# Kernel tuning notes

Measured on AMD Instinct MI355X. Metric: run time of the kernel, lower is better.

Reference implementation:

```python
import jax, jax.numpy as jnp
import numpy as np

NUM_NODES = 100000
NUM_REL = 8
HIDDEN = 128
NUM_EDGES = 1600000
NUM_LAYERS = 2


def setup_inputs() -> dict:
    key = jax.random.key(0)
    k1, k2, k3, k4, k5 = jax.random.split(key, 5)
    x = jnp.arange(NUM_NODES, dtype=jnp.int64)
    edge_index = jax.random.randint(k1, (2, NUM_EDGES), 0, NUM_NODES, dtype=jnp.int64)
    edge_type = jax.random.randint(k2, (NUM_EDGES,), 0, NUM_REL, dtype=jnp.int64)
    emb = jax.random.normal(k3, (NUM_NODES, HIDDEN), dtype=jnp.float32) * 0.1
    W = jax.random.normal(k4, (NUM_LAYERS, NUM_REL, HIDDEN, HIDDEN), dtype=jnp.float32) * (1.0 / np.sqrt(HIDDEN))
    root = jax.random.normal(k5, (NUM_LAYERS, HIDDEN, HIDDEN), dtype=jnp.float32) * (1.0 / np.sqrt(HIDDEN))
    bias = jnp.zeros((NUM_LAYERS, HIDDEN), dtype=jnp.float32)
    return {"x": x, "edge_index": edge_index, "edge_type": edge_type,
            "emb": emb, "W": W, "root": root, "bias": bias}


def _rgcn_conv(h, src, dst, etype, W_l, root_l, bias_l):
    # h: [N, d]; W_l: [R, d, d]
    n = h.shape[0]
    r = W_l.shape[0]
    # Transform all nodes by every relation weight: [R, N, d]
    xW = jnp.einsum('nd,rdf->rnf', h, W_l)
    # Per-edge message gathered by (relation, source): [E, d]
    msg = xW[etype, src]
    # Mean-normalize per (target node, relation), matching PyG aggr='mean'
    seg = dst * r + etype  # combined (node, relation) segment id
    cnt = jax.ops.segment_sum(jnp.ones(msg.shape[0], dtype=h.dtype), seg,
                              num_segments=n * r)
    norm = 1.0 / jnp.maximum(cnt[seg], 1.0)
    agg = jax.ops.segment_sum(msg * norm[:, None], dst, num_segments=n)
    return agg + h @ root_l + bias_l


def reference(x, edge_index, edge_type, emb, W, root, bias):
    src, dst = edge_index[0], edge_index[1]
    h = emb[x]  # embedding lookup
    for l in range(NUM_LAYERS):
        h = _rgcn_conv(h, src, dst, edge_type, W[l], root[l], bias[l])
        h = jax.nn.relu(h)
    return h
```

## Files before the change

kernel.cpp:

```cpp
#include <hip/hip_runtime.h>

typedef unsigned int u32;
typedef unsigned short u16;
typedef __attribute__((ext_vector_type(8))) short short8;
typedef __attribute__((ext_vector_type(4))) float f32x4;

#define DD 128
#define RREL 8
#define KCAT 1152
#define NKT 9
#define SCAN_CHUNK 4096

static __device__ __forceinline__ u16 f2bf(float f) {
  u32 u = __builtin_bit_cast(u32, f);
  u32 r = (u + 0x7fffu + ((u >> 16) & 1u)) >> 16;
  return (u16)r;
}
static __device__ __forceinline__ float bflo(u32 v) { return __builtin_bit_cast(float, v << 16); }
static __device__ __forceinline__ float bfhi(u32 v) { return __builtin_bit_cast(float, v & 0xffff0000u); }

__global__ __launch_bounds__(256) void k_convw(const float* __restrict__ W,
                                               const float* __restrict__ root,
                                               uint4* __restrict__ wt) {
  int t = blockIdx.x * 256 + threadIdx.x;
  if (t >= 2 * NKT * 2048) return;
  int l = t / (NKT * 2048);
  int rem = t - l * (NKT * 2048);
  int kt = rem >> 11;
  int pos = rem & 2047;
  int col = pos >> 4;
  int cbx = pos & 15;
  int cb = cbx ^ (col & 7);
  int k0 = kt * DD + cb * 8;
  u16 vals[8];
#pragma unroll
  for (int i = 0; i < 8; ++i) {
    int k = k0 + i;
    float v;
    if (k < DD) {
      v = root[(size_t)l * DD * DD + k * DD + col];
    } else {
      int km = k - DD;
      v = W[((size_t)l * RREL + (km >> 7)) * DD * DD + (size_t)(km & 127) * DD + col];
    }
    vals[i] = f2bf(v);
  }
  wt[t] = *(uint4*)vals;
}

__global__ __launch_bounds__(256) void k_gather(const int* __restrict__ x,
                                                const float* __restrict__ emb,
                                                u16* __restrict__ acat, int N) {
  int t = blockIdx.x * 256 + threadIdx.x;
  if (t >= N * 16) return;
  int node = t >> 4, part = t & 15;
  const float4* e4 = (const float4*)(emb + (size_t)x[node] * DD + part * 8);
  float4 f0 = e4[0], f1 = e4[1];
  uint4 u;
  u.x = (u32)f2bf(f0.x) | ((u32)f2bf(f0.y) << 16);
  u.y = (u32)f2bf(f0.z) | ((u32)f2bf(f0.w) << 16);
  u.z = (u32)f2bf(f1.x) | ((u32)f2bf(f1.y) << 16);
  u.w = (u32)f2bf(f1.z) | ((u32)f2bf(f1.w) << 16);
  *(uint4*)(acat + (size_t)node * KCAT + part * 8) = u;
}

__global__ __launch_bounds__(256) void k_hist(const int* __restrict__ ei,
                                              const int* __restrict__ et,
                                              int* __restrict__ cnt, int E) {
  int base = (blockIdx.x * 256 + threadIdx.x) * 8;
  if (base + 7 < E) {
    int4 dA = *(const int4*)(ei + E + base);
    int4 dB = *(const int4*)(ei + E + base + 4);
    int4 tA = *(const int4*)(et + base);
    int4 tB = *(const int4*)(et + base + 4);
    atomicAdd(&cnt[dA.x * 8 + tA.x], 1);
    atomicAdd(&cnt[dA.y * 8 + tA.y], 1);
    atomicAdd(&cnt[dA.z * 8 + tA.z], 1);
    atomicAdd(&cnt[dA.w * 8 + tA.w], 1);
    atomicAdd(&cnt[dB.x * 8 + tB.x], 1);
    atomicAdd(&cnt[dB.y * 8 + tB.y], 1);
    atomicAdd(&cnt[dB.z * 8 + tB.z], 1);
    atomicAdd(&cnt[dB.w * 8 + tB.w], 1);
  } else {
    for (int e = base; e < E; ++e) atomicAdd(&cnt[ei[E + e] * 8 + et[e]], 1);
  }
}

__global__ __launch_bounds__(256) void k_scan_reduce(const int* __restrict__ cnt,
                                                     int* __restrict__ blksum, int nseg) {
  __shared__ int s[256];
  int b = blockIdx.x, t = threadIdx.x;
  int base = b * SCAN_CHUNK;
  int sum = 0;
  for (int i = 0; i < 16; ++i) {
    int idx = base + i * 256 + t;
    if (idx < nseg) sum += cnt[idx];
  }
  s[t] = sum;
  __syncthreads();
  for (int st = 128; st > 0; st >>= 1) {
    if (t < st) s[t] += s[t + st];
    __syncthreads();
  }
  if (t == 0) blksum[b] = s[0];
}

__global__ void k_scan_top(int* __restrict__ blksum, int nblk, int* __restrict__ off,
                           int nseg, int E) {
  if (threadIdx.x == 0 && blockIdx.x == 0) {
    int run = 0;
    for (int b = 0; b < nblk; ++b) { int v = blksum[b]; blksum[b] = run; run += v; }
    off[nseg] = E;
  }
}

__global__ __launch_bounds__(256) void k_scan_write(const int* __restrict__ cnt,
                                                    const int* __restrict__ blksum,
                                                    int* __restrict__ off, int nseg) {
  __shared__ int s[256];
  int b = blockIdx.x, t = threadIdx.x;
  int base = b * SCAN_CHUNK + t * 16;
  int v[16];
  int sum = 0;
#pragma unroll
  for (int i = 0; i < 16; ++i) {
    int idx = base + i;
    v[i] = (idx < nseg) ? cnt[idx] : 0;
    sum += v[i];
  }
  s[t] = sum;
  __syncthreads();
  for (int st = 1; st < 256; st <<= 1) {
    int add = (t >= st) ? s[t - st] : 0;
    __syncthreads();
    s[t] += add;
    __syncthreads();
  }
  int run = blksum[b] + s[t] - sum;
#pragma unroll
  for (int i = 0; i < 16; ++i) {
    int idx = base + i;
    if (idx < nseg) off[idx] = run;
    run += v[i];
  }
}

__global__ __launch_bounds__(256) void k_scatter(const int* __restrict__ ei,
                                                 const int* __restrict__ et,
                                                 int* __restrict__ fill,
                                                 int* __restrict__ sorted, int E) {
  int base = (blockIdx.x * 256 + threadIdx.x) * 8;
  if (base + 7 < E) {
    int4 sA = *(const int4*)(ei + base);
    int4 sB = *(const int4*)(ei + base + 4);
    int4 dA = *(const int4*)(ei + E + base);
    int4 dB = *(const int4*)(ei + E + base + 4);
    int4 tA = *(const int4*)(et + base);
    int4 tB = *(const int4*)(et + base + 4);
    int p0 = atomicAdd(&fill[dA.x * 8 + tA.x], 1);
    int p1 = atomicAdd(&fill[dA.y * 8 + tA.y], 1);
    int p2 = atomicAdd(&fill[dA.z * 8 + tA.z], 1);
    int p3 = atomicAdd(&fill[dA.w * 8 + tA.w], 1);
    int p4 = atomicAdd(&fill[dB.x * 8 + tB.x], 1);
    int p5 = atomicAdd(&fill[dB.y * 8 + tB.y], 1);
    int p6 = atomicAdd(&fill[dB.z * 8 + tB.z], 1);
    int p7 = atomicAdd(&fill[dB.w * 8 + tB.w], 1);
    sorted[p0] = sA.x;
    sorted[p1] = sA.y;
    sorted[p2] = sA.z;
    sorted[p3] = sA.w;
    sorted[p4] = sB.x;
    sorted[p5] = sB.y;
    sorted[p6] = sB.z;
    sorted[p7] = sB.w;
  } else {
    for (int e = base; e < E; ++e) {
      int pos = atomicAdd(&fill[ei[E + e] * 8 + et[e]], 1);
      sorted[pos] = ei[e];
    }
  }
}

static __device__ __forceinline__ void add8(float* a, uint4 v) {
  a[0] += bflo(v.x); a[1] += bfhi(v.x);
  a[2] += bflo(v.y); a[3] += bfhi(v.y);
  a[4] += bflo(v.z); a[5] += bfhi(v.z);
  a[6] += bflo(v.w); a[7] += bfhi(v.w);
}

__global__ __launch_bounds__(256) void k_agg(const int* __restrict__ off,
                                             const int* __restrict__ sorted,
                                             u16* acat, int N, int E) {
  int wave = threadIdx.x >> 6, lane = threadIdx.x & 63;
  int grp = lane >> 3, oct = lane & 7;
  int dst = blockIdx.x * 32 + wave * 8 + grp;
  if (dst >= N) return;
  int4 b0 = *(const int4*)(off + dst * 8);
  int4 b1 = *(const int4*)(off + dst * 8 + 4);
  int je = off[dst * 8 + 8];
  int cs = b0.x;
  int e1 = b0.y, e2 = b0.z, e3 = b0.w, e4 = b1.x, e5 = b1.y, e6 = b1.z, e7 = b1.w, e8 = je;
  u16* ambase = acat + (size_t)dst * KCAT + DD + oct * 16;
  float a[16];
#pragma unroll
  for (int i = 0; i < 16; ++i) a[i] = 0.f;
  int j = cs;
  int r = 0;
  int lastidx = (E > 0) ? E - 1 : 0;
  while (true) {
    while (r < 8 && j >= e1) {
      int cnt = e1 - cs;
      float norm = (cnt > 0) ? 1.0f / (float)cnt : 0.f;
      uint4 w0, w1;
      w0.x = (u32)f2bf(a[0] * norm) | ((u32)f2bf(a[1] * norm) << 16);
      w0.y = (u32)f2bf(a[2] * norm) | ((u32)f2bf(a[3] * norm) << 16);
      w0.z = (u32)f2bf(a[4] * norm) | ((u32)f2bf(a[5] * norm) << 16);
      w0.w = (u32)f2bf(a[6] * norm) | ((u32)f2bf(a[7] * norm) << 16);
      w1.x = (u32)f2bf(a[8] * norm) | ((u32)f2bf(a[9] * norm) << 16);
      w1.y = (u32)f2bf(a[10] * norm) | ((u32)f2bf(a[11] * norm) << 16);
      w1.z = (u32)f2bf(a[12] * norm) | ((u32)f2bf(a[13] * norm) << 16);
      w1.w = (u32)f2bf(a[14] * norm) | ((u32)f2bf(a[15] * norm) << 16);
      uint4* outp = (uint4*)(ambase + (size_t)r * DD);
      outp[0] = w0;
      outp[1] = w1;
#pragma unroll
      for (int i = 0; i < 16; ++i) a[i] = 0.f;
      cs = e1;
      e1 = e2; e2 = e3; e3 = e4; e4 = e5; e5 = e6; e6 = e7; e7 = e8;
      ++r;
    }
    if (r >= 8) break;
    int j1 = j + 1;
    bool two = (j1 < e1);
    int s0 = sorted[j];
    int s1 = sorted[two ? j1 : lastidx];
    const uint4* p0 = (const uint4*)(acat + (size_t)s0 * KCAT + oct * 16);
    const uint4* p1 = (const uint4*)(acat + (size_t)s1 * KCAT + oct * 16);
    uint4 v0 = p0[0], v0b = p0[1];
    uint4 v1 = p1[0], v1b = p1[1];
    if (!two) {
      v1.x = v1.y = v1.z = v1.w = 0u;
      v1b.x = v1b.y = v1b.z = v1b.w = 0u;
    }
    add8(a, v0); add8(a + 8, v0b);
    add8(a, v1); add8(a + 8, v1b);
    j += two ? 2 : 1;
  }
}

template <bool LAST>
__global__ __launch_bounds__(512) void k_gemm(u16* acat, const uint4* __restrict__ wt,
                                              const float* __restrict__ bias,
                                              float* __restrict__ dout, int M) {
  __shared__ uint4 ldsB[2][2048];
  int tid = threadIdx.x, wave = tid >> 6, lane = tid & 63;
  int rowbase = blockIdx.x * 128 + wave * 16;
  int arow = rowbase + (lane & 15);
  int arc = arow < M ? arow : M - 1;
  int klane = (lane >> 4) << 3;
  f32x4 acc[8];
#pragma unroll
  for (int c = 0; c < 8; ++c) acc[c] = (f32x4)0.f;

#define STAGE(KT, BUF)                                                                   \
  do {                                                                                   \
    const uint4* gsrc = wt + (size_t)(KT) * 2048;                                        \
    _Pragma("unroll") for (int i_ = 0; i_ < 4; ++i_) {                                   \
      int cid_ = i_ * 512 + tid;                                                         \
      __builtin_amdgcn_global_load_lds(                                                  \
          (const __attribute__((address_space(1))) uint4*)(gsrc + cid_),                 \
          (__attribute__((address_space(3))) uint4*)&ldsB[BUF][cid_], 16, 0, 0);         \
    }                                                                                    \
  } while (0)

  STAGE(0, 0);
  for (int kt = 0; kt < NKT; ++kt) {
    int cur = kt & 1;
    __syncthreads();
    if (kt + 1 < NKT) STAGE(kt + 1, cur ^ 1);
#pragma unroll
    for (int kc = 0; kc < 4; ++kc) {
      short8 a = *(const short8*)(acat + (size_t)arc * KCAT + kt * DD + kc * 32 + klane);
      int chunk = kc * 4 + (lane >> 4);
#pragma unroll
      for (int c = 0; c < 8; ++c) {
        int col = c * 16 + (lane & 15);
        const short8* bp = (const short8*)&ldsB[cur][col * 16 + (chunk ^ (col & 7))];
        acc[c] = __builtin_amdgcn_mfma_f32_16x16x32_bf16(a, *bp, acc[c], 0, 0, 0);
      }
    }
  }
#undef STAGE

  int crow0 = rowbase + ((lane >> 4) << 2);
  int ccol = lane & 15;
#pragma unroll
  for (int c = 0; c < 8; ++c) {
    int col = c * 16 + ccol;
    float bv = bias[col];
#pragma unroll
    for (int i = 0; i < 4; ++i) {
      int row = crow0 + i;
      if (row < M) {
        float v = fmaxf(acc[c][i] + bv, 0.f);
        if (LAST) dout[(size_t)row * DD + col] = v;
        else acat[(size_t)row * KCAT + col] = f2bf(v);
      }
    }
  }
}

extern "C" void kernel_launch(void* const* d_in, const int* in_sizes, int n_in,
                              void* d_out, int out_size, void* d_ws, size_t ws_size,
                              hipStream_t stream) {
  const int* x = (const int*)d_in[0];
  const int* ei = (const int*)d_in[1];
  const int* et = (const int*)d_in[2];
  const float* emb = (const float*)d_in[3];
  const float* W = (const float*)d_in[4];
  const float* root = (const float*)d_in[5];
  const float* bias = (const float*)d_in[6];

  const int N = in_sizes[0];
  const int E = in_sizes[2];
  const int NSEG = N * RREL;

  size_t o = 0;
  auto al = [&](size_t b) { size_t r = o; o = (o + b + 255) & ~(size_t)255; return r; };
  size_t off_o = al(((size_t)NSEG + 1) * 4);
  size_t cnt_o = al((size_t)NSEG * 4);
  size_t fill_o = al((size_t)NSEG * 4);
  size_t sorted_o = al((size_t)E * 4);
  size_t blk_o = al(4096);
  size_t wt_o = al((size_t)2 * NKT * 2048 * 16);
  size_t acat_o = al((size_t)N * KCAT * 2);
  (void)acat_o;

  char* ws = (char*)d_ws;
  int* off = (int*)(ws + off_o);
  int* cnt = (int*)(ws + cnt_o);
  int* fill = (int*)(ws + fill_o);
  int* sorted = (int*)(ws + sorted_o);
  int* blks = (int*)(ws + blk_o);
  uint4* wt = (uint4*)(ws + wt_o);
  u16* acat = (u16*)(ws + acat_o);
  float* outf = (float*)d_out;

  k_convw<<<(2 * NKT * 2048 + 255) / 256, 256, 0, stream>>>(W, root, wt);
  k_gather<<<(N * 16 + 255) / 256, 256, 0, stream>>>(x, emb, acat, N);
  hipMemsetAsync(cnt, 0, (size_t)NSEG * 4, stream);
  int egrid = ((E + 7) / 8 + 255) / 256;
  k_hist<<<egrid, 256, 0, stream>>>(ei, et, cnt, E);
  int nblk = (NSEG + SCAN_CHUNK - 1) / SCAN_CHUNK;
  k_scan_reduce<<<nblk, 256, 0, stream>>>(cnt, blks, NSEG);
  k_scan_top<<<1, 64, 0, stream>>>(blks, nblk, off, NSEG, E);
  k_scan_write<<<nblk, 256, 0, stream>>>(cnt, blks, off, NSEG);
  hipMemcpyAsync(fill, off, (size_t)NSEG * 4, hipMemcpyDeviceToDevice, stream);
  k_scatter<<<egrid, 256, 0, stream>>>(ei, et, fill, sorted, E);

  int gx = (N + 127) / 128;
  int agrid = (N + 31) / 32;
  k_agg<<<agrid, 256, 0, stream>>>(off, sorted, acat, N, E);
  k_gemm<false><<<gx, 512, 0, stream>>>(acat, wt, bias, nullptr, N);
  k_agg<<<agrid, 256, 0, stream>>>(off, sorted, acat, N, E);
  k_gemm<true><<<gx, 512, 0, stream>>>(acat, wt + (size_t)NKT * 2048, bias + DD, outf, N);
}
```

Before: 554.5 us.

## Split node features into a compact hidden array and a separate aggregate buffer

Node features move out of the wide concatenated row (self features plus 8 relation aggregates) into a dense N×128 bf16 array. Aggregates go to their own N×1024 buffer, and the GEMM reads its first K tile from the compact array. This makes the random per-edge source gathers in the aggregation kernel hit a small contiguous array instead of rows strided by 2304 bytes, which should improve cache locality. The scan kernel also writes the fill offsets directly, removing a device-to-device memcpy. The histogram and scatter kernels now handle 4 edges per thread instead of 8.

After: 568.9 us. +2.6%, slower.

```diff
diff --git a/kernel.cpp b/kernel.cpp
--- a/kernel.cpp
+++ b/kernel.cpp
@@ -7,7 +7,7 @@
 
 #define DD 128
 #define RREL 8
-#define KCAT 1152
+#define AMW 1024
 #define NKT 9
 #define SCAN_CHUNK 4096
 
@@ -50,7 +50,7 @@
 
 __global__ __launch_bounds__(256) void k_gather(const int* __restrict__ x,
                                                 const float* __restrict__ emb,
-                                                u16* __restrict__ acat, int N) {
+                                                u16* __restrict__ h0, int N) {
   int t = blockIdx.x * 256 + threadIdx.x;
   if (t >= N * 16) return;
   int node = t >> 4, part = t & 15;
@@ -61,26 +61,20 @@
   u.y = (u32)f2bf(f0.z) | ((u32)f2bf(f0.w) << 16);
   u.z = (u32)f2bf(f1.x) | ((u32)f2bf(f1.y) << 16);
   u.w = (u32)f2bf(f1.z) | ((u32)f2bf(f1.w) << 16);
-  *(uint4*)(acat + (size_t)node * KCAT + part * 8) = u;
+  *(uint4*)(h0 + (size_t)node * DD + part * 8) = u;
 }
 
 __global__ __launch_bounds__(256) void k_hist(const int* __restrict__ ei,
                                               const int* __restrict__ et,
                                               int* __restrict__ cnt, int E) {
-  int base = (blockIdx.x * 256 + threadIdx.x) * 8;
-  if (base + 7 < E) {
-    int4 dA = *(const int4*)(ei + E + base);
-    int4 dB = *(const int4*)(ei + E + base + 4);
-    int4 tA = *(const int4*)(et + base);
-    int4 tB = *(const int4*)(et + base + 4);
-    atomicAdd(&cnt[dA.x * 8 + tA.x], 1);
-    atomicAdd(&cnt[dA.y * 8 + tA.y], 1);
-    atomicAdd(&cnt[dA.z * 8 + tA.z], 1);
-    atomicAdd(&cnt[dA.w * 8 + tA.w], 1);
-    atomicAdd(&cnt[dB.x * 8 + tB.x], 1);
-    atomicAdd(&cnt[dB.y * 8 + tB.y], 1);
-    atomicAdd(&cnt[dB.z * 8 + tB.z], 1);
-    atomicAdd(&cnt[dB.w * 8 + tB.w], 1);
+  int base = (blockIdx.x * 256 + threadIdx.x) * 4;
+  if (base + 3 < E) {
+    int4 d4 = *(const int4*)(ei + E + base);
+    int4 t4 = *(const int4*)(et + base);
+    atomicAdd(&cnt[d4.x * 8 + t4.x], 1);
+    atomicAdd(&cnt[d4.y * 8 + t4.y], 1);
+    atomicAdd(&cnt[d4.z * 8 + t4.z], 1);
+    atomicAdd(&cnt[d4.w * 8 + t4.w], 1);
   } else {
     for (int e = base; e < E; ++e) atomicAdd(&cnt[ei[E + e] * 8 + et[e]], 1);
   }
@@ -116,7 +110,8 @@
 
 __global__ __launch_bounds__(256) void k_scan_write(const int* __restrict__ cnt,
                                                     const int* __restrict__ blksum,
-                                                    int* __restrict__ off, int nseg) {
+                                                    int* __restrict__ off,
+                                                    int* __restrict__ fill, int nseg) {
   __shared__ int s[256];
   int b = blockIdx.x, t = threadIdx.x;
   int base = b * SCAN_CHUNK + t * 16;
@@ -140,7 +135,7 @@
 #pragma unroll
   for (int i = 0; i < 16; ++i) {
     int idx = base + i;
-    if (idx < nseg) off[idx] = run;
+    if (idx < nseg) { off[idx] = run; fill[idx] = run; }
     run += v[i];
   }
 }
@@ -149,30 +144,19 @@
                                                  const int* __restrict__ et,
                                                  int* __restrict__ fill,
                                                  int* __restrict__ sorted, int E) {
-  int base = (blockIdx.x * 256 + threadIdx.x) * 8;
-  if (base + 7 < E) {
-    int4 sA = *(const int4*)(ei + base);
-    int4 sB = *(const int4*)(ei + base + 4);
-    int4 dA = *(const int4*)(ei + E + base);
-    int4 dB = *(const int4*)(ei + E + base + 4);
-    int4 tA = *(const int4*)(et + base);
-    int4 tB = *(const int4*)(et + base + 4);
-    int p0 = atomicAdd(&fill[dA.x * 8 + tA.x], 1);
-    int p1 = atomicAdd(&fill[dA.y * 8 + tA.y], 1);
-    int p2 = atomicAdd(&fill[dA.z * 8 + tA.z], 1);
-    int p3 = atomicAdd(&fill[dA.w * 8 + tA.w], 1);
-    int p4 = atomicAdd(&fill[dB.x * 8 + tB.x], 1);
-    int p5 = atomicAdd(&fill[dB.y * 8 + tB.y], 1);
-    int p6 = atomicAdd(&fill[dB.z * 8 + tB.z], 1);
-    int p7 = atomicAdd(&fill[dB.w * 8 + tB.w], 1);
-    sorted[p0] = sA.x;
-    sorted[p1] = sA.y;
-    sorted[p2] = sA.z;
-    sorted[p3] = sA.w;
-    sorted[p4] = sB.x;
-    sorted[p5] = sB.y;
-    sorted[p6] = sB.z;
-    sorted[p7] = sB.w;
+  int base = (blockIdx.x * 256 + threadIdx.x) * 4;
+  if (base + 3 < E) {
+    int4 s4 = *(const int4*)(ei + base);
+    int4 d4 = *(const int4*)(ei + E + base);
+    int4 t4 = *(const int4*)(et + base);
+    int p0 = atomicAdd(&fill[d4.x * 8 + t4.x], 1);
+    int p1 = atomicAdd(&fill[d4.y * 8 + t4.y], 1);
+    int p2 = atomicAdd(&fill[d4.z * 8 + t4.z], 1);
+    int p3 = atomicAdd(&fill[d4.w * 8 + t4.w], 1);
+    sorted[p0] = s4.x;
+    sorted[p1] = s4.y;
+    sorted[p2] = s4.z;
+    sorted[p3] = s4.w;
   } else {
     for (int e = base; e < E; ++e) {
       int pos = atomicAdd(&fill[ei[E + e] * 8 + et[e]], 1);
@@ -190,7 +174,8 @@
 
 __global__ __launch_bounds__(256) void k_agg(const int* __restrict__ off,
                                              const int* __restrict__ sorted,
-                                             u16* acat, int N, int E) {
+                                             const u16* __restrict__ hin,
+                                             u16* __restrict__ am, int N, int E) {
   int wave = threadIdx.x >> 6, lane = threadIdx.x & 63;
   int grp = lane >> 3, oct = lane & 7;
   int dst = blockIdx.x * 32 + wave * 8 + grp;
@@ -200,7 +185,7 @@
   int je = off[dst * 8 + 8];
   int cs = b0.x;
   int e1 = b0.y, e2 = b0.z, e3 = b0.w, e4 = b1.x, e5 = b1.y, e6 = b1.z, e7 = b1.w, e8 = je;
-  u16* ambase = acat + (size_t)dst * KCAT + DD + oct * 16;
+  u16* ambase = am + (size_t)dst * AMW + oct * 16;
   float a[16];
 #pragma unroll
   for (int i = 0; i < 16; ++i) a[i] = 0.f;
@@ -234,8 +219,8 @@
     bool two = (j1 < e1);
     int s0 = sorted[j];
     int s1 = sorted[two ? j1 : lastidx];
-    const uint4* p0 = (const uint4*)(acat + (size_t)s0 * KCAT + oct * 16);
-    const uint4* p1 = (const uint4*)(acat + (size_t)s1 * KCAT + oct * 16);
+    const uint4* p0 = (const uint4*)(hin + (size_t)s0 * DD + oct * 16);
+    const uint4* p1 = (const uint4*)(hin + (size_t)s1 * DD + oct * 16);
     uint4 v0 = p0[0], v0b = p0[1];
     uint4 v1 = p1[0], v1b = p1[1];
     if (!two) {
@@ -249,8 +234,11 @@
 }
 
 template <bool LAST>
-__global__ __launch_bounds__(512) void k_gemm(u16* acat, const uint4* __restrict__ wt,
+__global__ __launch_bounds__(512) void k_gemm(const u16* __restrict__ h,
+                                              const u16* __restrict__ am,
+                                              const uint4* __restrict__ wt,
                                               const float* __restrict__ bias,
+                                              u16* __restrict__ hout,
                                               float* __restrict__ dout, int M) {
   __shared__ uint4 ldsB[2][2048];
   int tid = threadIdx.x, wave = tid >> 6, lane = tid & 63;
@@ -278,9 +266,11 @@
     int cur = kt & 1;
     __syncthreads();
     if (kt + 1 < NKT) STAGE(kt + 1, cur ^ 1);
+    const u16* abase = (kt == 0) ? (h + (size_t)arc * DD)
+                                 : (am + (size_t)arc * AMW + (kt - 1) * DD);
 #pragma unroll
     for (int kc = 0; kc < 4; ++kc) {
-      short8 a = *(const short8*)(acat + (size_t)arc * KCAT + kt * DD + kc * 32 + klane);
+      short8 a = *(const short8*)(abase + kc * 32 + klane);
       int chunk = kc * 4 + (lane >> 4);
 #pragma unroll
       for (int c = 0; c < 8; ++c) {
@@ -304,7 +294,7 @@
       if (row < M) {
         float v = fmaxf(acc[c][i] + bv, 0.f);
         if (LAST) dout[(size_t)row * DD + col] = v;
-        else acat[(size_t)row * KCAT + col] = f2bf(v);
+        else hout[(size_t)row * DD + col] = f2bf(v);
       }
     }
   }
@@ -333,8 +323,9 @@
   size_t sorted_o = al((size_t)E * 4);
   size_t blk_o = al(4096);
   size_t wt_o = al((size_t)2 * NKT * 2048 * 16);
-  size_t acat_o = al((size_t)N * KCAT * 2);
-  (void)acat_o;
+  size_t h0_o = al((size_t)N * DD * 2);
+  size_t am_o = al((size_t)N * AMW * 2);
+  (void)am_o;
 
   char* ws = (char*)d_ws;
   int* off = (int*)(ws + off_o);
@@ -343,25 +334,25 @@
   int* sorted = (int*)(ws + sorted_o);
   int* blks = (int*)(ws + blk_o);
   uint4* wt = (uint4*)(ws + wt_o);
-  u16* acat = (u16*)(ws + acat_o);
+  u16* h0 = (u16*)(ws + h0_o);
+  u16* am = (u16*)(ws + am_o);
   float* outf = (float*)d_out;
 
   k_convw<<<(2 * NKT * 2048 + 255) / 256, 256, 0, stream>>>(W, root, wt);
-  k_gather<<<(N * 16 + 255) / 256, 256, 0, stream>>>(x, emb, acat, N);
+  k_gather<<<(N * 16 + 255) / 256, 256, 0, stream>>>(x, emb, h0, N);
   hipMemsetAsync(cnt, 0, (size_t)NSEG * 4, stream);
-  int egrid = ((E + 7) / 8 + 255) / 256;
-  k_hist<<<egrid, 256, 0, stream>>>(ei, et, cnt, E);
+  k_hist<<<((E + 3) / 4 + 255) / 256, 256, 0, stream>>>(ei, et, cnt, E);
   int nblk = (NSEG + SCAN_CHUNK - 1) / SCAN_CHUNK;
   k_scan_reduce<<<nblk, 256, 0, stream>>>(cnt, blks, NSEG);
   k_scan_top<<<1, 64, 0, stream>>>(blks, nblk, off, NSEG, E);
-  k_scan_write<<<nblk, 256, 0, stream>>>(cnt, blks, off, NSEG);
-  hipMemcpyAsync(fill, off, (size_t)NSEG * 4, hipMemcpyDeviceToDevice, stream);
-  k_scatter<<<egrid, 256, 0, stream>>>(ei, et, fill, sorted, E);
+  k_scan_write<<<nblk, 256, 0, stream>>>(cnt, blks, off, fill, NSEG);
+  k_scatter<<<((E + 3) / 4 + 255) / 256, 256, 0, stream>>>(ei, et, fill, sorted, E);
 
   int gx = (N + 127) / 128;
   int agrid = (N + 31) / 32;
-  k_agg<<<agrid, 256, 0, stream>>>(off, sorted, acat, N, E);
-  k_gemm<false><<<gx, 512, 0, stream>>>(acat, wt, bias, nullptr, N);
-  k_agg<<<agrid, 256, 0, stream>>>(off, sorted, acat, N, E);
-  k_gemm<true><<<gx, 512, 0, stream>>>(acat, wt + (size_t)NKT * 2048, bias + DD, outf, N);
-}
+  k_agg<<<agrid, 256, 0, stream>>>(off, sorted, h0, am, N, E);
+  k_gemm<false><<<gx, 512, 0, stream>>>(h0, am, wt, bias, h0, nullptr, N);
+  k_agg<<<agrid, 256, 0, stream>>>(off, sorted, h0, am, N, E);
+  k_gemm<true><<<gx, 512, 0, stream>>>(h0, am, wt + (size_t)NKT * 2048, bias + DD,
+                                       nullptr, outf, N);
+}
```
